# Kernel optimization log

Hardware: AMD Instinct MI355X
Metric: run time of the kernel (lower is better)

## Reference

```python
import jax, jax.numpy as jnp
import numpy as np

B = 524288   # particles
H = 128      # hidden_size
E = 64       # embed_dim
NT = 512     # num trajectories
IN = 16 + 9 + E  # fc1 input dim = 89
EPS = 1e-6


def setup_inputs() -> dict:
    key = jax.random.key(0)
    ks = jax.random.split(key, 12)
    w = lambda k, shp, fan_in: (jax.random.normal(k, shp, dtype=jnp.float32)
                                / np.sqrt(fan_in).astype(np.float32))
    return {
        "F": jax.random.normal(ks[0], (B, 3, 3), dtype=jnp.float32),
        "C": jax.random.normal(ks[1], (B, 3, 3), dtype=jnp.float32),
        "traj_id": 7,
        "latent": jax.random.normal(ks[2], (NT, E), dtype=jnp.float32),
        "W1": w(ks[3], (IN, H), IN), "b1": jnp.zeros((H,), jnp.float32),
        "W2": w(ks[4], (H, H), H),   "b2": jnp.zeros((H,), jnp.float32),
        "W3": w(ks[5], (H, H), H),   "b3": jnp.zeros((H,), jnp.float32),
        "W4": w(ks[6], (H, H), H),   "b4": jnp.zeros((H,), jnp.float32),
        "W5": w(ks[7], (H, H), H),   "b5": jnp.zeros((H,), jnp.float32),
        "W6": w(ks[8], (H, H), H),   "b6": jnp.zeros((H,), jnp.float32),
        "W7": w(ks[9], (H, 9), H),   "b7": jnp.zeros((9,), jnp.float32),
    }


def _strain_features(F):
    # FFt: [B,3,3]; J = clamp(det F); J1 = clamp(F00); sigma: 3 singular values
    FFt = jnp.einsum('bij,bkj->bik', F, F)
    J = jnp.maximum(jnp.linalg.det(F), EPS)
    J1 = jnp.maximum(F[:, 0, 0], EPS)
    sigma = jnp.linalg.svd(F, compute_uv=False)  # descending, like torch.svd
    return jnp.concatenate([
        FFt.reshape(-1, 9),
        jnp.log(J)[:, None], sigma, J[:, None],
        jnp.log(J1)[:, None], J1[:, None],
    ], axis=-1)  # [B,16]


def reference(F, C, traj_id, latent,
              W1, b1, W2, b2, W3, b3, W4, b4, W5, b5, W6, b6, W7, b7):
    strain = _strain_features(F)                                   # [B,16]
    lat = jnp.broadcast_to(latent[traj_id], (F.shape[0], latent.shape[1]))
    x = jnp.concatenate([strain, C.reshape(-1, 9), lat], axis=-1)  # [B,89]
    g = lambda z: jax.nn.gelu(z, approximate=False)  # exact, matches torch GELU
    x = g(x @ W1 + b1)
    x = g(x @ W2 + b2)
    x = g(x @ W3 + b3)
    x = g(x @ W4 + b4)
    x = g(x @ W5 + b5)
    x = g(x @ W6 + b6)
    out = (x @ W7 + b7).reshape(-1, 3, 3)
    return 0.5 * (out + jnp.swapaxes(out, 1, 2))  # symmetric stress [B,3,3]
```

## Files before the change

### kernel.cpp

```cpp
#include <hip/hip_runtime.h>
#include <hip/hip_bf16.h>
#include <math.h>

#define BPART   524288
#define NBLK    (BPART / 128)
#define W7_OFF  98304
#define WB_N    102400
#define BIAS_N  800
#define PREP_N  (WB_N + BIAS_N)

typedef __bf16 bf16x8 __attribute__((ext_vector_type(8)));
typedef float  f32x16 __attribute__((ext_vector_type(16)));
typedef float  f32x4  __attribute__((ext_vector_type(4)));
typedef float  f32x2  __attribute__((ext_vector_type(2)));

#define MFMA __builtin_amdgcn_mfma_f32_32x32x16_bf16

__device__ __forceinline__ unsigned short f2bf(float f) {
  union { float f; unsigned u; } v; v.f = f;
  unsigned r = v.u + 0x7fffu + ((v.u >> 16) & 1u);
  return (unsigned short)(r >> 16);
}
__device__ __forceinline__ unsigned pack_bf16(float a, float b) {
  unsigned ua = __builtin_bit_cast(unsigned, a) + 0x8000u;
  unsigned ub = __builtin_bit_cast(unsigned, b) + 0x8000u;
  return __builtin_amdgcn_perm(ub, ua, 0x07060302u);
}
__device__ __forceinline__ int swz(int row, int col) {
  return (row << 7) | ((((col >> 3) ^ (row & 7)) << 3) | (col & 7));
}

__device__ __forceinline__ f32x2 pk_mul(f32x2 a, f32x2 b) {
  f32x2 d; asm("v_pk_mul_f32 %0, %1, %2" : "=v"(d) : "v"(a), "v"(b)); return d;
}
__device__ __forceinline__ f32x2 pk_fma(f32x2 a, f32x2 b, f32x2 c) {
  f32x2 d; asm("v_pk_fma_f32 %0, %1, %2, %3" : "=v"(d) : "v"(a), "v"(b), "v"(c)); return d;
}
__device__ __forceinline__ f32x2 gelu2(f32x2 z) {
  const f32x2 c1 = {0.1029432f, 0.1029432f};
  const f32x2 c0 = {2.30220818f, 2.30220818f};
  f32x2 z2 = pk_mul(z, z);
  f32x2 t  = pk_fma(z2, c1, c0);
  f32x2 yp = pk_mul(z, t);
  float e0 = __builtin_amdgcn_exp2f(-yp.x);
  float e1 = __builtin_amdgcn_exp2f(-yp.y);
  float r0 = __builtin_amdgcn_rcpf(e0 + 1.0f);
  float r1 = __builtin_amdgcn_rcpf(e1 + 1.0f);
  f32x2 g; g.x = z.x * r0; g.y = z.y * r1;
  return g;
}
__device__ __forceinline__ void cp16(const void* g, void* l) {
  __builtin_amdgcn_global_load_lds(
      (const __attribute__((address_space(1))) void*)g,
      (__attribute__((address_space(3))) void*)l, 16, 0, 0);
}

__global__ void prep_weights(
    const float* __restrict__ W1, const float* __restrict__ W2,
    const float* __restrict__ W3, const float* __restrict__ W4,
    const float* __restrict__ W5, const float* __restrict__ W6,
    const float* __restrict__ W7,
    const float* __restrict__ b1, const float* __restrict__ b2,
    const float* __restrict__ b3, const float* __restrict__ b4,
    const float* __restrict__ b5, const float* __restrict__ b6,
    const float* __restrict__ b7,
    unsigned short* __restrict__ wsb, float* __restrict__ wsf)
{
  int idx = blockIdx.x * 256 + threadIdx.x;
  if (idx < WB_N) {
    unsigned short v = 0;
    if (idx < W7_OFF) {
      int l = idx >> 14;
      int o = idx & 16383;
      int n = o >> 7, e = o & 127;
      int k = (((e >> 3) ^ (n & 7)) << 3) | (e & 7);
      const float* W = (l==0)?W1:(l==1)?W2:(l==2)?W3:(l==3)?W4:(l==4)?W5:W6;
      float x = (l == 0) ? ((k < 89) ? W[k*128 + n] : 0.0f)
                         : W[k*128 + n];
      v = f2bf(x);
    } else {
      int o = idx - W7_OFF;
      int n = o >> 7, e = o & 127;
      int k = (((e >> 3) ^ (n & 7)) << 3) | (e & 7);
      v = (n < 9) ? f2bf(W7[k*9 + n]) : (unsigned short)0;
    }
    wsb[idx] = v;
  } else if (idx < PREP_N) {
    int r = idx - WB_N;
    float x;
    if (r < 768) {
      int l = r >> 7, n = r & 127;
      const float* bb = (l==0)?b1:(l==1)?b2:(l==2)?b3:(l==3)?b4:(l==4)?b5:b6;
      x = bb[n];
    } else {
      int n = r - 768;
      x = (n < 9) ? b7[n] : 0.0f;
    }
    wsf[r] = x;
  }
}

__global__ __launch_bounds__(256, 2) void stress_mlp(
    const float* __restrict__ F, const float* __restrict__ Cmat,
    const int* __restrict__ traj, const float* __restrict__ latent,
    const unsigned short* __restrict__ wst, const float* __restrict__ wsf,
    float* __restrict__ out)
{
  __shared__ __align__(16) unsigned short act_s[128 * 128];
  __shared__ __align__(16) unsigned short wt_s[128 * 128];

  const int tid  = threadIdx.x;
  const int lane = tid & 63;
  const int wid  = tid >> 6;
  const int lm   = lane & 31;
  const int lk   = lane >> 5;
  const int m0   = (wid >> 1) << 6;
  const int n0   = (wid & 1) << 6;
  const int pbase = (int)blockIdx.x << 7;

  {
    const char* src = (const char*)wst;
    char* dst = (char*)wt_s;
    #pragma unroll
    for (int i = 0; i < 8; ++i)
      cp16(src + i*4096 + tid*16, dst + i*4096 + tid*16);
  }

  if (tid < 128) {
    const int row = tid;
    const int p   = pbase + row;
    float f[9];
    #pragma unroll
    for (int i = 0; i < 9; ++i) f[i] = F[p * 9 + i];
    float fft[9];
    #pragma unroll
    for (int i = 0; i < 3; ++i)
      #pragma unroll
      for (int k = 0; k < 3; ++k)
        fft[i*3+k] = f[i*3]*f[k*3] + f[i*3+1]*f[k*3+1] + f[i*3+2]*f[k*3+2];
    float det = f[0]*(f[4]*f[8]-f[5]*f[7]) - f[1]*(f[3]*f[8]-f[5]*f[6])
              + f[2]*(f[3]*f[7]-f[4]*f[6]);
    float J  = fmaxf(det, 1e-6f);
    float J1 = fmaxf(f[0], 1e-6f);
    float a00=fft[0], a01=fft[1], a02=fft[2], a11=fft[4], a12=fft[5], a22=fft[8];
    float q  = (a00+a11+a22) * (1.0f/3.0f);
    float d0 = a00-q, d1 = a11-q, d2 = a22-q;
    float p2 = d0*d0 + d1*d1 + d2*d2 + 2.0f*(a01*a01 + a02*a02 + a12*a12);
    float e0, e1, e2;
    if (p2 < 1e-14f) { e0 = e1 = e2 = q; }
    else {
      float pp  = sqrtf(p2 * (1.0f/6.0f));
      float inv = 1.0f / pp;
      float b00=d0*inv, b11=d1*inv, b22=d2*inv, b01=a01*inv, b02=a02*inv, b12=a12*inv;
      float detb = b00*(b11*b22-b12*b12) - b01*(b01*b22-b12*b02) + b02*(b01*b12-b11*b02);
      float rr = 0.5f * detb;
      rr = fminf(fmaxf(rr, -1.0f), 1.0f);
      float pr = acosf(rr) * (1.0f / (3.0f * 6.2831853071795864f));
      e0 = q + 2.0f*pp*__builtin_amdgcn_cosf(pr);
      e2 = q + 2.0f*pp*__builtin_amdgcn_cosf(pr + (1.0f/3.0f));
      e1 = 3.0f*q - e0 - e2;
    }
    float s0 = sqrtf(fmaxf(e0, 0.f));
    float s1 = sqrtf(fmaxf(e1, 0.f));
    float s2 = sqrtf(fmaxf(e2, 0.f));
    #pragma unroll
    for (int i = 0; i < 9; ++i) act_s[swz(row, i)] = f2bf(fft[i]);
    act_s[swz(row,  9)] = f2bf(logf(J));
    act_s[swz(row, 10)] = f2bf(s0);
    act_s[swz(row, 11)] = f2bf(s1);
    act_s[swz(row, 12)] = f2bf(s2);
    act_s[swz(row, 13)] = f2bf(J);
    act_s[swz(row, 14)] = f2bf(logf(J1));
    act_s[swz(row, 15)] = f2bf(J1);
    #pragma unroll
    for (int i = 0; i < 9; ++i) act_s[swz(row, 16 + i)] = f2bf(Cmat[p*9 + i]);
  } else {
    const int row = tid - 128;
    const int t = traj[0];
    const float* lat = latent + t * 64;
    for (int j = 0; j < 64; ++j) act_s[swz(row, 25 + j)] = f2bf(lat[j]);
    for (int j = 89; j < 128; ++j) act_s[swz(row, j)] = 0;
  }

  const int mr0 = m0 + lm,      mr1 = m0 + 32 + lm;
  const int nr0 = n0 + lm,      nr1 = n0 + 32 + lm;

  f32x16 acc[2][2];
  union BF { f32x16 v; f32x4 q[4]; };

  for (int l = 0; l < 6; ++l) {
    BF bias[2];
    const float* bl = wsf + (l << 7);
    #pragma unroll
    for (int tn = 0; tn < 2; ++tn)
      #pragma unroll
      for (int qq = 0; qq < 4; ++qq)
        bias[tn].q[qq] = *(const f32x4*)(bl + n0 + (tn << 5) + (qq << 3) + (lk << 2));

    __syncthreads();

    {
      bf16x8 x0 = *(const bf16x8*)&act_s[(mr0 << 7) + ((lk ^ (mr0 & 7)) << 3)];
      bf16x8 x1 = *(const bf16x8*)&act_s[(mr1 << 7) + ((lk ^ (mr1 & 7)) << 3)];
      bf16x8 w0 = *(const bf16x8*)&wt_s[(nr0 << 7) + ((lk ^ (nr0 & 7)) << 3)];
      bf16x8 w1 = *(const bf16x8*)&wt_s[(nr1 << 7) + ((lk ^ (nr1 & 7)) << 3)];
      acc[0][0] = MFMA(w0, x0, bias[0].v, 0, 0, 0);
      acc[0][1] = MFMA(w0, x1, bias[0].v, 0, 0, 0);
      acc[1][0] = MFMA(w1, x0, bias[1].v, 0, 0, 0);
      acc[1][1] = MFMA(w1, x1, bias[1].v, 0, 0, 0);
    }
    #pragma unroll
    for (int kk = 1; kk < 8; ++kk) {
      const int kc = (kk << 1) + lk;
      bf16x8 x0 = *(const bf16x8*)&act_s[(mr0 << 7) + ((kc ^ (mr0 & 7)) << 3)];
      bf16x8 x1 = *(const bf16x8*)&act_s[(mr1 << 7) + ((kc ^ (mr1 & 7)) << 3)];
      bf16x8 w0 = *(const bf16x8*)&wt_s[(nr0 << 7) + ((kc ^ (nr0 & 7)) << 3)];
      bf16x8 w1 = *(const bf16x8*)&wt_s[(nr1 << 7) + ((kc ^ (nr1 & 7)) << 3)];
      acc[0][0] = MFMA(w0, x0, acc[0][0], 0, 0, 0);
      acc[0][1] = MFMA(w0, x1, acc[0][1], 0, 0, 0);
      acc[1][0] = MFMA(w1, x0, acc[1][0], 0, 0, 0);
      acc[1][1] = MFMA(w1, x1, acc[1][1], 0, 0, 0);
    }
    __syncthreads();

    if (l < 5) {
      const char* src = (const char*)(wst + ((l + 1) << 14));
      char* dst = (char*)wt_s;
      #pragma unroll
      for (int i = 0; i < 8; ++i)
        cp16(src + i*4096 + tid*16, dst + i*4096 + tid*16);
    } else {
      const char* src = (const char*)(wst + W7_OFF);
      char* dst = (char*)wt_s;
      #pragma unroll
      for (int i = 0; i < 2; ++i)
        cp16(src + i*4096 + tid*16, dst + i*4096 + tid*16);
    }

    #pragma unroll
    for (int tm = 0; tm < 2; ++tm) {
      const int m    = m0 + (tm << 5) + lm;
      const int rowb = m << 7;
      const int rx   = m & 7;
      #pragma unroll
      for (int tn = 0; tn < 2; ++tn) {
        const int cb = ((n0 + (tn << 5)) >> 3);
        #pragma unroll
        for (int q = 0; q < 4; ++q) {
          f32x2 za; za.x = acc[tn][tm][4*q + 0]; za.y = acc[tn][tm][4*q + 1];
          f32x2 zb; zb.x = acc[tn][tm][4*q + 2]; zb.y = acc[tn][tm][4*q + 3];
          f32x2 ga = gelu2(za);
          f32x2 gb = gelu2(zb);
          uint2 u;
          u.x = pack_bf16(ga.x, ga.y);
          u.y = pack_bf16(gb.x, gb.y);
          const int off = rowb + (((cb + q) ^ rx) << 3) + (lk << 2);
          *reinterpret_cast<uint2*>(&act_s[off]) = u;
        }
      }
    }
  }

  {
    BF bias7;
    #pragma unroll
    for (int qq = 0; qq < 4; ++qq)
      bias7.q[qq] = *(const f32x4*)(wsf + 768 + (qq << 3) + (lk << 2));

    __syncthreads();

    f32x16 acc7[2];
    if ((wid & 1) == 0) {
      {
        bf16x8 x0 = *(const bf16x8*)&act_s[(mr0 << 7) + ((lk ^ (mr0 & 7)) << 3)];
        bf16x8 x1 = *(const bf16x8*)&act_s[(mr1 << 7) + ((lk ^ (mr1 & 7)) << 3)];
        bf16x8 w0 = *(const bf16x8*)&wt_s[(lm << 7) + ((lk ^ (lm & 7)) << 3)];
        acc7[0] = MFMA(w0, x0, bias7.v, 0, 0, 0);
        acc7[1] = MFMA(w0, x1, bias7.v, 0, 0, 0);
      }
      #pragma unroll
      for (int kk = 1; kk < 8; ++kk) {
        const int kc = (kk << 1) + lk;
        bf16x8 x0 = *(const bf16x8*)&act_s[(mr0 << 7) + ((kc ^ (mr0 & 7)) << 3)];
        bf16x8 x1 = *(const bf16x8*)&act_s[(mr1 << 7) + ((kc ^ (mr1 & 7)) << 3)];
        bf16x8 w0 = *(const bf16x8*)&wt_s[(lm << 7) + ((kc ^ (lm & 7)) << 3)];
        acc7[0] = MFMA(w0, x0, acc7[0], 0, 0, 0);
        acc7[1] = MFMA(w0, x1, acc7[1], 0, 0, 0);
      }
    }
    __syncthreads();

    float* ots = (float*)wt_s;
    if ((wid & 1) == 0) {
      #pragma unroll
      for (int tm = 0; tm < 2; ++tm) {
        const int m = m0 + (tm << 5) + lm;
        #pragma unroll
        for (int j = 0; j < 4; ++j)
          ots[m * 9 + (lk << 2) + j] = acc7[tm][j];
        if (lk == 0) ots[m * 9 + 8] = acc7[tm][4];
      }
    }
    __syncthreads();

    if (tid < 128) {
      const int row = tid;
      float z[9];
      #pragma unroll
      for (int i = 0; i < 9; ++i) z[i] = ots[row * 9 + i];
      #pragma unroll
      for (int rr = 0; rr < 3; ++rr)
        #pragma unroll
        for (int cc = 0; cc < 3; ++cc)
          ots[row * 9 + rr*3 + cc] = 0.5f * (z[rr*3+cc] + z[cc*3+rr]);
    }
    __syncthreads();

    float4* dst = (float4*)(out + (size_t)pbase * 9);
    const float4* srcv = (const float4*)ots;
    for (int s = tid; s < 288; s += 256) dst[s] = srcv[s];
  }
}

extern "C" void kernel_launch(void* const* d_in, const int* in_sizes, int n_in,
                              void* d_out, int out_size, void* d_ws, size_t ws_size,
                              hipStream_t stream) {
  const float* F   = (const float*)d_in[0];
  const float* C   = (const float*)d_in[1];
  const int*   trj = (const int*)d_in[2];
  const float* lat = (const float*)d_in[3];
  const float* W1  = (const float*)d_in[4];
  const float* b1  = (const float*)d_in[5];
  const float* W2  = (const float*)d_in[6];
  const float* b2  = (const float*)d_in[7];
  const float* W3  = (const float*)d_in[8];
  const float* b3  = (const float*)d_in[9];
  const float* W4  = (const float*)d_in[10];
  const float* b4  = (const float*)d_in[11];
  const float* W5  = (const float*)d_in[12];
  const float* b5  = (const float*)d_in[13];
  const float* W6  = (const float*)d_in[14];
  const float* b6  = (const float*)d_in[15];
  const float* W7  = (const float*)d_in[16];
  const float* b7  = (const float*)d_in[17];

  unsigned short* wsb = (unsigned short*)d_ws;
  float* wsf = (float*)((char*)d_ws + WB_N * 2);

  prep_weights<<<dim3((PREP_N + 255) / 256), dim3(256), 0, stream>>>(
      W1, W2, W3, W4, W5, W6, W7, b1, b2, b3, b4, b5, b6, b7, wsb, wsf);
  stress_mlp<<<dim3(NBLK), dim3(256), 0, stream>>>(
      F, C, trj, lat, wsb, wsf, (float*)d_out);
}
```

Baseline: 287.9 us.

## Read MLP weights directly from global/L2 instead of staging in LDS

Removes the shared-memory weight buffer and its async global-to-LDS copies, and reorders the prepared bf16 weight layout so each lane's 8-element K chunk is contiguous in global memory. The MFMA loop now loads weight fragments straight from global memory, relying on L2/L1 caching. This halves LDS use per block, which may allow higher occupancy, and drops the LDS copy traffic. The cost is global-load latency inside the inner MFMA loop and an extra barrier per layer.

```diff
diff --git a/kernel.cpp b/kernel.cpp
--- a/kernel.cpp
+++ b/kernel.cpp
@@ -48,11 +48,6 @@
   float r1 = __builtin_amdgcn_rcpf(e1 + 1.0f);
   f32x2 g; g.x = z.x * r0; g.y = z.y * r1;
   return g;
-}
-__device__ __forceinline__ void cp16(const void* g, void* l) {
-  __builtin_amdgcn_global_load_lds(
-      (const __attribute__((address_space(1))) void*)g,
-      (__attribute__((address_space(3))) void*)l, 16, 0, 0);
 }
 
 __global__ void prep_weights(
@@ -70,18 +65,22 @@
   if (idx < WB_N) {
     unsigned short v = 0;
     if (idx < W7_OFF) {
-      int l = idx >> 14;
-      int o = idx & 16383;
-      int n = o >> 7, e = o & 127;
-      int k = (((e >> 3) ^ (n & 7)) << 3) | (e & 7);
+      int l  = idx >> 14;
+      int o  = idx & 16383;
+      int j  = o & 7;
+      int n  = (o >> 3) & 127;
+      int kc = o >> 10;
+      int k  = (kc << 3) | j;
       const float* W = (l==0)?W1:(l==1)?W2:(l==2)?W3:(l==3)?W4:(l==4)?W5:W6;
       float x = (l == 0) ? ((k < 89) ? W[k*128 + n] : 0.0f)
                          : W[k*128 + n];
       v = f2bf(x);
     } else {
-      int o = idx - W7_OFF;
-      int n = o >> 7, e = o & 127;
-      int k = (((e >> 3) ^ (n & 7)) << 3) | (e & 7);
+      int o  = idx - W7_OFF;
+      int j  = o & 7;
+      int n  = (o >> 3) & 31;
+      int kc = o >> 8;
+      int k  = (kc << 3) | j;
       v = (n < 9) ? f2bf(W7[k*9 + n]) : (unsigned short)0;
     }
     wsb[idx] = v;
@@ -107,7 +106,6 @@
     float* __restrict__ out)
 {
   __shared__ __align__(16) unsigned short act_s[128 * 128];
-  __shared__ __align__(16) unsigned short wt_s[128 * 128];
 
   const int tid  = threadIdx.x;
   const int lane = tid & 63;
@@ -117,14 +115,6 @@
   const int m0   = (wid >> 1) << 6;
   const int n0   = (wid & 1) << 6;
   const int pbase = (int)blockIdx.x << 7;
-
-  {
-    const char* src = (const char*)wst;
-    char* dst = (char*)wt_s;
-    #pragma unroll
-    for (int i = 0; i < 8; ++i)
-      cp16(src + i*4096 + tid*16, dst + i*4096 + tid*16);
-  }
 
   if (tid < 128) {
     const int row = tid;
@@ -188,6 +178,8 @@
   f32x16 acc[2][2];
   union BF { f32x16 v; f32x4 q[4]; };
 
+  __syncthreads();
+
   for (int l = 0; l < 6; ++l) {
     BF bias[2];
     const float* bl = wsf + (l << 7);
@@ -197,13 +189,14 @@
       for (int qq = 0; qq < 4; ++qq)
         bias[tn].q[qq] = *(const f32x4*)(bl + n0 + (tn << 5) + (qq << 3) + (lk << 2));
 
-    __syncthreads();
+    const unsigned short* wl = wst + (l << 14);
 
     {
-      bf16x8 x0 = *(const bf16x8*)&act_s[(mr0 << 7) + ((lk ^ (mr0 & 7)) << 3)];
-      bf16x8 x1 = *(const bf16x8*)&act_s[(mr1 << 7) + ((lk ^ (mr1 & 7)) << 3)];
-      bf16x8 w0 = *(const bf16x8*)&wt_s[(nr0 << 7) + ((lk ^ (nr0 & 7)) << 3)];
-      bf16x8 w1 = *(const bf16x8*)&wt_s[(nr1 << 7) + ((lk ^ (nr1 & 7)) << 3)];
+      const int kc = lk;
+      bf16x8 x0 = *(const bf16x8*)&act_s[(mr0 << 7) + ((kc ^ (mr0 & 7)) << 3)];
+      bf16x8 x1 = *(const bf16x8*)&act_s[(mr1 << 7) + ((kc ^ (mr1 & 7)) << 3)];
+      bf16x8 w0 = *(const bf16x8*)(wl + (((kc << 7) + nr0) << 3));
+      bf16x8 w1 = *(const bf16x8*)(wl + (((kc << 7) + nr1) << 3));
       acc[0][0] = MFMA(w0, x0, bias[0].v, 0, 0, 0);
       acc[0][1] = MFMA(w0, x1, bias[0].v, 0, 0, 0);
       acc[1][0] = MFMA(w1, x0, bias[1].v, 0, 0, 0);
@@ -214,28 +207,14 @@
       const int kc = (kk << 1) + lk;
       bf16x8 x0 = *(const bf16x8*)&act_s[(mr0 << 7) + ((kc ^ (mr0 & 7)) << 3)];
       bf16x8 x1 = *(const bf16x8*)&act_s[(mr1 << 7) + ((kc ^ (mr1 & 7)) << 3)];
-      bf16x8 w0 = *(const bf16x8*)&wt_s[(nr0 << 7) + ((kc ^ (nr0 & 7)) << 3)];
-      bf16x8 w1 = *(const bf16x8*)&wt_s[(nr1 << 7) + ((kc ^ (nr1 & 7)) << 3)];
+      bf16x8 w0 = *(const bf16x8*)(wl + (((kc << 7) + nr0) << 3));
+      bf16x8 w1 = *(const bf16x8*)(wl + (((kc << 7) + nr1) << 3));
       acc[0][0] = MFMA(w0, x0, acc[0][0], 0, 0, 0);
       acc[0][1] = MFMA(w0, x1, acc[0][1], 0, 0, 0);
       acc[1][0] = MFMA(w1, x0, acc[1][0], 0, 0, 0);
       acc[1][1] = MFMA(w1, x1, acc[1][1], 0, 0, 0);
     }
     __syncthreads();
-
-    if (l < 5) {
-      const char* src = (const char*)(wst + ((l + 1) << 14));
-      char* dst = (char*)wt_s;
-      #pragma unroll
-      for (int i = 0; i < 8; ++i)
-        cp16(src + i*4096 + tid*16, dst + i*4096 + tid*16);
-    } else {
-      const char* src = (const char*)(wst + W7_OFF);
-      char* dst = (char*)wt_s;
-      #pragma unroll
-      for (int i = 0; i < 2; ++i)
-        cp16(src + i*4096 + tid*16, dst + i*4096 + tid*16);
-    }
 
     #pragma unroll
     for (int tm = 0; tm < 2; ++tm) {
@@ -259,22 +238,23 @@
         }
       }
     }
+    __syncthreads();
   }
 
   {
-    BF bias7;
-    #pragma unroll
-    for (int qq = 0; qq < 4; ++qq)
-      bias7.q[qq] = *(const f32x4*)(wsf + 768 + (qq << 3) + (lk << 2));
-
-    __syncthreads();
-
     f32x16 acc7[2];
+    const unsigned short* w7 = wst + W7_OFF;
+
     if ((wid & 1) == 0) {
+      BF bias7;
+      #pragma unroll
+      for (int qq = 0; qq < 4; ++qq)
+        bias7.q[qq] = *(const f32x4*)(wsf + 768 + (qq << 3) + (lk << 2));
       {
-        bf16x8 x0 = *(const bf16x8*)&act_s[(mr0 << 7) + ((lk ^ (mr0 & 7)) << 3)];
-        bf16x8 x1 = *(const bf16x8*)&act_s[(mr1 << 7) + ((lk ^ (mr1 & 7)) << 3)];
-        bf16x8 w0 = *(const bf16x8*)&wt_s[(lm << 7) + ((lk ^ (lm & 7)) << 3)];
+        const int kc = lk;
+        bf16x8 x0 = *(const bf16x8*)&act_s[(mr0 << 7) + ((kc ^ (mr0 & 7)) << 3)];
+        bf16x8 x1 = *(const bf16x8*)&act_s[(mr1 << 7) + ((kc ^ (mr1 & 7)) << 3)];
+        bf16x8 w0 = *(const bf16x8*)(w7 + (((kc << 5) + lm) << 3));
         acc7[0] = MFMA(w0, x0, bias7.v, 0, 0, 0);
         acc7[1] = MFMA(w0, x1, bias7.v, 0, 0, 0);
       }
@@ -283,14 +263,14 @@
         const int kc = (kk << 1) + lk;
         bf16x8 x0 = *(const bf16x8*)&act_s[(mr0 << 7) + ((kc ^ (mr0 & 7)) << 3)];
         bf16x8 x1 = *(const bf16x8*)&act_s[(mr1 << 7) + ((kc ^ (mr1 & 7)) << 3)];
-        bf16x8 w0 = *(const bf16x8*)&wt_s[(lm << 7) + ((kc ^ (lm & 7)) << 3)];
+        bf16x8 w0 = *(const bf16x8*)(w7 + (((kc << 5) + lm) << 3));
         acc7[0] = MFMA(w0, x0, acc7[0], 0, 0, 0);
         acc7[1] = MFMA(w0, x1, acc7[1], 0, 0, 0);
       }
     }
     __syncthreads();
 
-    float* ots = (float*)wt_s;
+    float* ots = (float*)act_s;
     if ((wid & 1) == 0) {
       #pragma unroll
       for (int tm = 0; tm < 2; ++tm) {
```

New measurement: 301.8 us. 1.05x slower.
